# Kernel optimization log

Hardware: AMD Instinct MI355X
Metric: run time of the kernel (lower is better)

## Reference

```python
import jax, jax.numpy as jnp
import numpy as np

L, D, OC, GROUPS, EPS = 256, 1280, 128, 8, 1e-5


def setup_inputs() -> dict:
    key = jax.random.key(0)
    k1, k2 = jax.random.split(key)
    feats = jax.random.normal(k1, (L, D), dtype=jnp.float32)
    # Conv2d(3d, out_ch, kernel_size=1) weight flattened to (out_ch, 3d)
    W = jax.random.normal(k2, (OC, 3 * D), dtype=jnp.float32) * (1.0 / np.sqrt(3 * D))
    b = jnp.zeros((OC,), dtype=jnp.float32)
    gamma = jnp.ones((OC,), dtype=jnp.float32)
    beta = jnp.zeros((OC,), dtype=jnp.float32)
    return {"feats": feats, "W": W, "b": b, "gamma": gamma, "beta": beta}


def reference(feats, W, b, gamma, beta):
    fi = feats[:, None, :]                     # (L, 1, d)
    fj = feats[None, :, :]                     # (1, L, d)
    add = fi + fj                              # (L, L, d)
    diff = jnp.abs(fi - fj)                    # (L, L, d)
    had = fi * fj                              # (L, L, d)
    pair = jnp.concatenate([add, diff, had], axis=-1)  # (L, L, 3d)
    # 1x1 conv == per-pixel linear: (L, L, 3d) x (out_ch, 3d)^T -> (L, L, out_ch)
    x = jnp.einsum('ijc,oc->ijo', pair, W) + b
    # GroupNorm(8, out_ch) on batch=1: normalize over (C/g, L, L) per group
    xg = jnp.transpose(x, (2, 0, 1)).reshape(GROUPS, OC // GROUPS, L, L)
    mean = jnp.mean(xg, axis=(1, 2, 3), keepdims=True)
    var = jnp.var(xg, axis=(1, 2, 3), keepdims=True)
    xn = ((xg - mean) * jax.lax.rsqrt(var + EPS)).reshape(OC, L, L)
    xn = xn * gamma[:, None, None] + beta[:, None, None]
    out = jax.nn.gelu(xn, approximate=False)   # torch nn.GELU default = exact erf
    return out[None]                           # (1, out_ch, L, L)
```

## Files before the change

kernel.cpp:

```cpp
#include <hip/hip_runtime.h>
#include <math.h>

typedef unsigned int uint;
typedef unsigned short ushort;

typedef __attribute__((ext_vector_type(8))) _Float16 f16x8;
typedef __attribute__((ext_vector_type(2))) _Float16 f16x2;
typedef __attribute__((ext_vector_type(16))) float floatx16;

#define NFEAT 327680
#define NWA   163840
#define NWP   327680

union U4H8 { uint4 u; f16x8 h; uint w[4]; };

__device__ inline ushort f2h(float f) {
  _Float16 h = (_Float16)f;
  union { _Float16 h; ushort s; } c; c.h = h; return c.s;
}
__device__ inline f16x2 asf16x2(uint u) {
  union { uint u; f16x2 h; } c; c.u = u; return c.h;
}
__device__ inline uint asuint(f16x2 h) {
  union { f16x2 h; uint u; } c; c.h = h; return c.u;
}

__global__ void prep_kernel(const float* __restrict__ feats,
                            const float* __restrict__ W,
                            ushort* __restrict__ fH,
                            ushort* __restrict__ wA,
                            ushort* __restrict__ wP,
                            float* __restrict__ stats,
                            float* __restrict__ Aoi) {
  int idx = blockIdx.x * 256 + threadIdx.x;
  if (blockIdx.x == 0 && threadIdx.x < 16) stats[threadIdx.x] = 0.0f;
  if (idx < 32768) Aoi[idx] = 0.0f;
  if (idx < NFEAT) {
    fH[idx] = f2h(feats[idx]);
  } else {
    const int e = idx - NFEAT;
    const int o = e / 3840;
    const int c = e - o * 3840;
    const ushort v = f2h(W[e]);
    if (c < 1280) {
      wA[o * 1280 + c] = v;
    } else {
      const int cp = c - 1280;
      const int t = cp / 1280;
      const int kk = cp - t * 1280;
      const int ks = kk >> 4;
      const int khalf = (kk >> 3) & 1;
      const int ko = kk & 7;
      const int lane = khalf * 32 + (o & 31);
      const int tile = (ks * 2 + t) * 4 + (o >> 5);
      wP[tile * 512 + lane * 8 + ko] = v;
    }
  }
}

__global__ __launch_bounds__(256, 2) void gemma_kernel(
    const ushort* __restrict__ fH, const ushort* __restrict__ wA,
    float* __restrict__ Aoi) {
  __shared__ float red[4][1024];
  const int tid = threadIdx.x, lane = tid & 63, w = tid >> 6;
  const int i0 = (blockIdx.x >> 4) << 5;
  const int kq = (blockIdx.x >> 2) & 3;
  const int ot = blockIdx.x & 3;
  const int rr = lane & 31, half = lane >> 5;
  floatx16 a4;
  #pragma unroll
  for (int r = 0; r < 16; ++r) a4[r] = 0.0f;
  const int kbase = kq * 320 + w * 80 + half * 8;
  #pragma unroll
  for (int ks = 0; ks < 5; ++ks) {
    const int k = kbase + ks * 16;
    U4H8 bf; bf.u = *(const uint4*)(fH + (i0 + rr) * 1280 + k);
    U4H8 af; af.u = *(const uint4*)(wA + (ot * 32 + rr) * 1280 + k);
    a4 = __builtin_amdgcn_mfma_f32_32x32x16_f16(af.h, bf.h, a4, 0, 0, 0);
  }
  #pragma unroll
  for (int r = 0; r < 16; ++r) {
    const int orow = (r & 3) + 8 * (r >> 2) + 4 * half;
    red[w][orow * 32 + rr] = a4[r];
  }
  __syncthreads();
  for (int e = tid; e < 1024; e += 256) {
    float s = red[0][e] + red[1][e] + red[2][e] + red[3][e];
    atomicAdd(&Aoi[(ot * 32 + (e >> 5)) * 256 + i0 + (e & 31)], s);
  }
}

__device__ inline void build_pair(const uint4 vj, const uint4 vi, U4H8& d, U4H8& h) {
  const uint ju[4] = {vj.x, vj.y, vj.z, vj.w};
  const uint iu[4] = {vi.x, vi.y, vi.z, vi.w};
  #pragma unroll
  for (int t = 0; t < 4; ++t) {
    f16x2 a = asf16x2(iu[t]);
    f16x2 b = asf16x2(ju[t]);
    f16x2 dd = a - b;
    f16x2 hh = a * b;
    d.w[t] = asuint(dd) & 0x7fff7fffu;
    h.w[t] = asuint(hh);
  }
}

__global__ __launch_bounds__(256, 1) void gemm_kernel(
    const ushort* __restrict__ fH, const ushort* __restrict__ wP,
    const float* __restrict__ bias, const float* __restrict__ Aoi,
    float* __restrict__ xout, float* __restrict__ stats) {
  __shared__ float sred[16];

  const int tid = threadIdx.x;
  const int blk = blockIdx.x;
  const int lane = tid & 63;
  const int w = tid >> 6;
  const int ip = w >> 1;
  const int ot = w & 1;
  const int i0 = (blk >> 2) * 4 + ip * 2;
  const int j0 = (blk & 3) << 6;
  const int wo = ot << 6;
  const int rr = lane & 31;
  const int half = lane >> 5;

  const ushort* wpl = wP + ((wo >> 5) << 9) + lane * 8;
  const ushort* fi0p = fH + i0 * 1280 + half * 8;
  const ushort* fi1p = fi0p + 1280;
  const ushort* fj0p = fH + (j0 + rr) * 1280 + half * 8;
  const ushort* fj1p = fj0p + 32 * 1280;

  floatx16 acc[2][2][2];
  #pragma unroll
  for (int a = 0; a < 2; ++a)
    #pragma unroll
    for (int b = 0; b < 2; ++b)
      #pragma unroll
      for (int c = 0; c < 2; ++c)
        #pragma unroll
        for (int r = 0; r < 16; ++r) acc[a][b][c][r] = 0.0f;

  U4H8 wfA[8], wfB[8];
  uint4 vj0A[2], vj1A[2], vi0A[2], vi1A[2];
  uint4 vj0B[2], vj1B[2], vi0B[2], vi1B[2];

#define CHUNK_LOAD(WF, VJ0, VJ1, VI0, VI1, CC) do {                           \
    const int _b = (CC) * 16;                                                 \
    _Pragma("unroll")                                                         \
    for (int _q = 0; _q < 8; ++_q) {                                          \
      const int _st = _q >> 2, _t = (_q >> 1) & 1, _oi = _q & 1;              \
      (WF)[_q].u = *(const uint4*)(wpl + ((_b + _st * 8 + _t * 4 + _oi) << 9)); \
    }                                                                         \
    const int _cb = (CC) << 5;                                                \
    _Pragma("unroll")                                                         \
    for (int _s = 0; _s < 2; ++_s) {                                          \
      (VJ0)[_s] = *(const uint4*)(fj0p + _cb + _s * 16);                      \
      (VJ1)[_s] = *(const uint4*)(fj1p + _cb + _s * 16);                      \
      (VI0)[_s] = *(const uint4*)(fi0p + _cb + _s * 16);                      \
      (VI1)[_s] = *(const uint4*)(fi1p + _cb + _s * 16);                      \
    }                                                                         \
  } while (0)

#define CHUNK_COMPUTE(WF, VJ0, VJ1, VI0, VI1) do {                            \
    _Pragma("unroll")                                                         \
    for (int _s = 0; _s < 2; ++_s) {                                          \
      U4H8 d00, h00, d01, h01, d10, h10, d11, h11;                            \
      build_pair((VJ0)[_s], (VI0)[_s], d00, h00);                             \
      build_pair((VJ0)[_s], (VI1)[_s], d01, h01);                             \
      build_pair((VJ1)[_s], (VI0)[_s], d10, h10);                             \
      build_pair((VJ1)[_s], (VI1)[_s], d11, h11);                             \
      _Pragma("unroll")                                                       \
      for (int _oi = 0; _oi < 2; ++_oi) {                                     \
        const f16x8 wd = (WF)[_s * 4 + _oi].h;                                \
        const f16x8 wh = (WF)[_s * 4 + 2 + _oi].h;                            \
        acc[0][0][_oi] = __builtin_amdgcn_mfma_f32_32x32x16_f16(wd, d00.h, acc[0][0][_oi], 0, 0, 0); \
        acc[1][0][_oi] = __builtin_amdgcn_mfma_f32_32x32x16_f16(wd, d01.h, acc[1][0][_oi], 0, 0, 0); \
        acc[0][1][_oi] = __builtin_amdgcn_mfma_f32_32x32x16_f16(wd, d10.h, acc[0][1][_oi], 0, 0, 0); \
        acc[1][1][_oi] = __builtin_amdgcn_mfma_f32_32x32x16_f16(wd, d11.h, acc[1][1][_oi], 0, 0, 0); \
        acc[0][0][_oi] = __builtin_amdgcn_mfma_f32_32x32x16_f16(wh, h00.h, acc[0][0][_oi], 0, 0, 0); \
        acc[1][0][_oi] = __builtin_amdgcn_mfma_f32_32x32x16_f16(wh, h01.h, acc[1][0][_oi], 0, 0, 0); \
        acc[0][1][_oi] = __builtin_amdgcn_mfma_f32_32x32x16_f16(wh, h10.h, acc[0][1][_oi], 0, 0, 0); \
        acc[1][1][_oi] = __builtin_amdgcn_mfma_f32_32x32x16_f16(wh, h11.h, acc[1][1][_oi], 0, 0, 0); \
      }                                                                       \
    }                                                                         \
  } while (0)

  CHUNK_LOAD(wfA, vj0A, vj1A, vi0A, vi1A, 0);
  #pragma unroll 1
  for (int cc = 0; cc < 40; cc += 2) {
    CHUNK_LOAD(wfB, vj0B, vj1B, vi0B, vi1B, cc + 1);
    CHUNK_COMPUTE(wfA, vj0A, vj1A, vi0A, vi1A);
    if (cc + 2 < 40)
      CHUNK_LOAD(wfA, vj0A, vj1A, vi0A, vi1A, cc + 2);
    CHUNK_COMPUTE(wfB, vj0B, vj1B, vi0B, vi1B);
  }
#undef CHUNK_LOAD
#undef CHUNK_COMPUTE

  float gs[2][2] = {{0.f, 0.f}, {0.f, 0.f}};
  float gq[2][2] = {{0.f, 0.f}, {0.f, 0.f}};
  #pragma unroll
  for (int ii = 0; ii < 2; ++ii) {
    const int irow = i0 + ii;
    #pragma unroll
    for (int js = 0; js < 2; ++js) {
      const int jg = j0 + js * 32 + rr;
      const int mglob = irow * 256 + jg;
      #pragma unroll
      for (int oi = 0; oi < 2; ++oi) {
        #pragma unroll
        for (int r = 0; r < 16; ++r) {
          const int orow = (r & 3) + 8 * (r >> 2) + 4 * half;
          const int o = wo + oi * 32 + orow;
          float x = acc[ii][js][oi][r] + Aoi[o * 256 + irow] + Aoi[o * 256 + jg] + bias[o];
          xout[o * 65536 + mglob] = x;
          gs[oi][r >> 3] += x;
          gq[oi][r >> 3] += x * x;
        }
      }
    }
  }
  if (tid < 16) sred[tid] = 0.0f;
  __syncthreads();
  #pragma unroll
  for (int oi = 0; oi < 2; ++oi) {
    #pragma unroll
    for (int rg = 0; rg < 2; ++rg) {
      float s = gs[oi][rg], qv = gq[oi][rg];
      for (int off = 32; off > 0; off >>= 1) {
        s += __shfl_xor(s, off, 64);
        qv += __shfl_xor(qv, off, 64);
      }
      if (lane == 0) {
        const int g = (wo >> 4) + oi * 2 + rg;
        atomicAdd(&sred[g], s);
        atomicAdd(&sred[8 + g], qv);
      }
    }
  }
  __syncthreads();
  if (tid < 16) atomicAdd(&stats[tid], sred[tid]);
}

__global__ void norm_kernel(float* __restrict__ xout,
                            const float* __restrict__ stats,
                            const float* __restrict__ gamma,
                            const float* __restrict__ beta) {
  const int idx = blockIdx.x * 256 + threadIdx.x;
  const int e = idx << 2;
  const int o = e >> 16;
  const int g = o >> 4;
  const float invN = 1.0f / 1048576.0f;
  const float mean = stats[g] * invN;
  const float var = stats[8 + g] * invN - mean * mean;
  const float inv = rsqrtf(var + 1e-5f);
  const float ga = gamma[o], be = beta[o];
  float4 v = *(float4*)(xout + e);
  float* pv = &v.x;
  #pragma unroll
  for (int t = 0; t < 4; ++t) {
    float xn = (pv[t] - mean) * inv * ga + be;
    pv[t] = 0.5f * xn * (1.0f + erff(xn * 0.70710678118654752f));
  }
  *(float4*)(xout + e) = v;
}

extern "C" void kernel_launch(void* const* d_in, const int* in_sizes, int n_in,
                              void* d_out, int out_size, void* d_ws, size_t ws_size,
                              hipStream_t stream) {
  const float* feats = (const float*)d_in[0];
  const float* W     = (const float*)d_in[1];
  const float* bias  = (const float*)d_in[2];
  const float* gamma = (const float*)d_in[3];
  const float* beta  = (const float*)d_in[4];
  float* out = (float*)d_out;

  ushort* fH = (ushort*)d_ws;
  ushort* wA = fH + NFEAT;
  ushort* wP = wA + NWA;
  float* stats = (float*)(wP + NWP);
  float* Aoi = stats + 16;

  prep_kernel<<<3200, 256, 0, stream>>>(feats, W, fH, wA, wP, stats, Aoi);
  gemma_kernel<<<128, 256, 0, stream>>>(fH, wA, Aoi);
  gemm_kernel<<<256, 256, 0, stream>>>(fH, wP, bias, Aoi, out, stats);
  norm_kernel<<<8192, 256, 0, stream>>>(out, stats, gamma, beta);
}
```

Before: 146.6 us.

## Fuse prep and Aoi GEMM into one launch reading fp32 directly

Merges the conversion/prep kernel and the small A·feats GEMM into a single launch. The first 32 blocks compute the Aoi partial product straight from fp32 feats and W, converting in registers. Each block now covers the full K range, so the result is stored plainly instead of via atomics, and no zero-init is needed. This removes one kernel launch, the wA staging buffer and the atomic traffic. In exchange the 32 GEMM blocks do four times more serial K work each, with uncoalesced scalar fp32 loads.

Result: slower. 153.4 us (+4.6%).

```diff
diff --git a/kernel.cpp b/kernel.cpp
--- a/kernel.cpp
+++ b/kernel.cpp
@@ -9,7 +9,6 @@
 typedef __attribute__((ext_vector_type(16))) float floatx16;
 
 #define NFEAT 327680
-#define NWA   163840
 #define NWP   327680
 
 union U4H8 { uint4 u; f16x8 h; uint w[4]; };
@@ -24,58 +23,59 @@
 __device__ inline uint asuint(f16x2 h) {
   union { f16x2 h; uint u; } c; c.h = h; return c.u;
 }
-
-__global__ void prep_kernel(const float* __restrict__ feats,
-                            const float* __restrict__ W,
-                            ushort* __restrict__ fH,
-                            ushort* __restrict__ wA,
-                            ushort* __restrict__ wP,
-                            float* __restrict__ stats,
-                            float* __restrict__ Aoi) {
-  int idx = blockIdx.x * 256 + threadIdx.x;
-  if (blockIdx.x == 0 && threadIdx.x < 16) stats[threadIdx.x] = 0.0f;
-  if (idx < 32768) Aoi[idx] = 0.0f;
-  if (idx < NFEAT) {
-    fH[idx] = f2h(feats[idx]);
-  } else {
-    const int e = idx - NFEAT;
-    const int o = e / 3840;
-    const int c = e - o * 3840;
-    const ushort v = f2h(W[e]);
-    if (c < 1280) {
-      wA[o * 1280 + c] = v;
+__device__ inline f16x8 cvt8(const float* p) {
+  f16x8 r;
+  #pragma unroll
+  for (int e = 0; e < 8; ++e) r[e] = (_Float16)p[e];
+  return r;
+}
+
+__global__ __launch_bounds__(256) void prep_gemma_kernel(
+    const float* __restrict__ feats, const float* __restrict__ W,
+    ushort* __restrict__ fH, ushort* __restrict__ wP,
+    float* __restrict__ stats, float* __restrict__ Aoi) {
+  __shared__ float red[4][1024];
+  const int bid = blockIdx.x;
+  const int tid = threadIdx.x;
+
+  if (bid >= 32) {
+    if (bid == 32 && tid < 16) stats[tid] = 0.0f;
+    const int idx = (bid - 32) * 256 + tid;
+    if (idx < NFEAT) {
+      fH[idx] = f2h(feats[idx]);
     } else {
-      const int cp = c - 1280;
-      const int t = cp / 1280;
-      const int kk = cp - t * 1280;
-      const int ks = kk >> 4;
-      const int khalf = (kk >> 3) & 1;
-      const int ko = kk & 7;
-      const int lane = khalf * 32 + (o & 31);
-      const int tile = (ks * 2 + t) * 4 + (o >> 5);
-      wP[tile * 512 + lane * 8 + ko] = v;
+      const int e = idx - NFEAT;
+      const int o = e / 3840;
+      const int c = e - o * 3840;
+      if (c >= 1280) {
+        const int cp = c - 1280;
+        const int t = cp / 1280;
+        const int kk = cp - t * 1280;
+        const int ks = kk >> 4;
+        const int khalf = (kk >> 3) & 1;
+        const int ko = kk & 7;
+        const int lane = khalf * 32 + (o & 31);
+        const int tile = (ks * 2 + t) * 4 + (o >> 5);
+        wP[tile * 512 + lane * 8 + ko] = f2h(W[e]);
+      }
     }
-  }
-}
-
-__global__ __launch_bounds__(256, 2) void gemma_kernel(
-    const ushort* __restrict__ fH, const ushort* __restrict__ wA,
-    float* __restrict__ Aoi) {
-  __shared__ float red[4][1024];
-  const int tid = threadIdx.x, lane = tid & 63, w = tid >> 6;
-  const int i0 = (blockIdx.x >> 4) << 5;
-  const int kq = (blockIdx.x >> 2) & 3;
-  const int ot = blockIdx.x & 3;
+    return;
+  }
+
+  const int lane = tid & 63, w = tid >> 6;
+  const int i0 = (bid >> 2) << 5;
+  const int ot = bid & 3;
   const int rr = lane & 31, half = lane >> 5;
   floatx16 a4;
   #pragma unroll
   for (int r = 0; r < 16; ++r) a4[r] = 0.0f;
-  const int kbase = kq * 320 + w * 80 + half * 8;
-  #pragma unroll
-  for (int ks = 0; ks < 5; ++ks) {
+  const int kbase = w * 320 + half * 8;
+  #pragma unroll
+  for (int ks = 0; ks < 20; ++ks) {
     const int k = kbase + ks * 16;
-    U4H8 bf; bf.u = *(const uint4*)(fH + (i0 + rr) * 1280 + k);
-    U4H8 af; af.u = *(const uint4*)(wA + (ot * 32 + rr) * 1280 + k);
+    U4H8 bf, af;
+    bf.h = cvt8(feats + (i0 + rr) * 1280 + k);
+    af.h = cvt8(W + (ot * 32 + rr) * 3840 + k);
     a4 = __builtin_amdgcn_mfma_f32_32x32x16_f16(af.h, bf.h, a4, 0, 0, 0);
   }
   #pragma unroll
@@ -86,7 +86,7 @@
   __syncthreads();
   for (int e = tid; e < 1024; e += 256) {
     float s = red[0][e] + red[1][e] + red[2][e] + red[3][e];
-    atomicAdd(&Aoi[(ot * 32 + (e >> 5)) * 256 + i0 + (e & 31)], s);
+    Aoi[(ot * 32 + (e >> 5)) * 256 + i0 + (e & 31)] = s;
   }
 }
 
@@ -274,13 +274,11 @@
   float* out = (float*)d_out;
 
   ushort* fH = (ushort*)d_ws;
-  ushort* wA = fH + NFEAT;
-  ushort* wP = wA + NWA;
+  ushort* wP = fH + NFEAT;
   float* stats = (float*)(wP + NWP);
   float* Aoi = stats + 16;
 
-  prep_kernel<<<3200, 256, 0, stream>>>(feats, W, fH, wA, wP, stats, Aoi);
-  gemma_kernel<<<128, 256, 0, stream>>>(fH, wA, Aoi);
+  prep_gemma_kernel<<<3232, 256, 0, stream>>>(feats, W, fH, wP, stats, Aoi);
   gemm_kernel<<<256, 256, 0, stream>>>(fH, wP, bias, Aoi, out, stats);
   norm_kernel<<<8192, 256, 0, stream>>>(out, stats, gamma, beta);
 }
```

## Exploit pair symmetry to compute only upper block-triangle and mirror outputs

Applied to the files above, without the earlier changes.

Since the pairwise features are symmetric in i and j, the GEMM now computes only tiles in the block upper triangle (plus diagonal blocks) and writes off-diagonal results to both (i,j) and (j,i), weighting them twice in the GroupNorm statistics. Blocks are reorganized as single-wave workgroups indexed over variable-size bands, and the LDS reduction is replaced by direct global atomics. This removes roughly a third of the MFMA work at the cost of uncoalesced transposed stores and more global atomics.

After: 257.8 us. 75.8% more time.

```diff
diff --git a/kernel.cpp b/kernel.cpp
--- a/kernel.cpp
+++ b/kernel.cpp
@@ -104,20 +104,21 @@
   }
 }
 
-__global__ __launch_bounds__(256, 1) void gemm_kernel(
+__global__ __launch_bounds__(64, 2) void gemm_kernel(
     const ushort* __restrict__ fH, const ushort* __restrict__ wP,
     const float* __restrict__ bias, const float* __restrict__ Aoi,
     float* __restrict__ xout, float* __restrict__ stats) {
-  __shared__ float sred[16];
-
-  const int tid = threadIdx.x;
+  const int lane = threadIdx.x;
   const int blk = blockIdx.x;
-  const int lane = tid & 63;
-  const int w = tid >> 6;
-  const int ip = w >> 1;
-  const int ot = w & 1;
-  const int i0 = (blk >> 2) * 4 + ip * 2;
-  const int j0 = (blk & 3) << 6;
+  const int tp = blk >> 1;
+  const int ot = blk & 1;
+  int band, base;
+  if (tp < 32)       { band = 0; base = 0; }
+  else if (tp < 96)  { band = 1; base = 32; }
+  else if (tp < 192) { band = 2; base = 96; }
+  else               { band = 3; base = 192; }
+  const int i0 = (tp - base) * 2;
+  const int j0 = band << 6;
   const int wo = ot << 6;
   const int rr = lane & 31;
   const int half = lane >> 5;
@@ -200,10 +201,12 @@
   #pragma unroll
   for (int ii = 0; ii < 2; ++ii) {
     const int irow = i0 + ii;
+    const int jdrop = (irow & ~63) + 64;
     #pragma unroll
     for (int js = 0; js < 2; ++js) {
       const int jg = j0 + js * 32 + rr;
-      const int mglob = irow * 256 + jg;
+      const bool mdrop = (jg & ~1) >= jdrop;
+      const float wt = mdrop ? 2.0f : 1.0f;
       #pragma unroll
       for (int oi = 0; oi < 2; ++oi) {
         #pragma unroll
@@ -211,15 +214,14 @@
           const int orow = (r & 3) + 8 * (r >> 2) + 4 * half;
           const int o = wo + oi * 32 + orow;
           float x = acc[ii][js][oi][r] + Aoi[o * 256 + irow] + Aoi[o * 256 + jg] + bias[o];
-          xout[o * 65536 + mglob] = x;
-          gs[oi][r >> 3] += x;
-          gq[oi][r >> 3] += x * x;
+          xout[o * 65536 + irow * 256 + jg] = x;
+          if (mdrop) xout[o * 65536 + jg * 256 + irow] = x;
+          gs[oi][r >> 3] += wt * x;
+          gq[oi][r >> 3] += wt * x * x;
         }
       }
     }
   }
-  if (tid < 16) sred[tid] = 0.0f;
-  __syncthreads();
   #pragma unroll
   for (int oi = 0; oi < 2; ++oi) {
     #pragma unroll
@@ -231,13 +233,11 @@
       }
       if (lane == 0) {
         const int g = (wo >> 4) + oi * 2 + rg;
-        atomicAdd(&sred[g], s);
-        atomicAdd(&sred[8 + g], qv);
+        atomicAdd(&stats[g], s);
+        atomicAdd(&stats[8 + g], qv);
       }
     }
   }
-  __syncthreads();
-  if (tid < 16) atomicAdd(&stats[tid], sred[tid]);
 }
 
 __global__ void norm_kernel(float* __restrict__ xout,
@@ -281,6 +281,6 @@
 
   prep_kernel<<<3200, 256, 0, stream>>>(feats, W, fH, wA, wP, stats, Aoi);
   gemma_kernel<<<128, 256, 0, stream>>>(fH, wA, Aoi);
-  gemm_kernel<<<256, 256, 0, stream>>>(fH, wP, bias, Aoi, out, stats);
+  gemm_kernel<<<640, 64, 0, stream>>>(fH, wP, bias, Aoi, out, stats);
   norm_kernel<<<8192, 256, 0, stream>>>(out, stats, gamma, beta);
 }
```
